# Kernel tuning notes

Measured on AMD Instinct MI355X. Metric: run time of the kernel, lower is better.

The kernel has to match this reference:

```python
import jax, jax.numpy as jnp
import numpy as np


def setup_inputs() -> dict:
    key = jax.random.key(0)
    ks = jax.random.split(key, 4)
    B, S, D, E = 8, 4096, 2048, 64
    scale = 1.0 / np.sqrt(D)
    return {
        "x": jax.random.normal(ks[0], (B, S, D), dtype=jnp.float32),
        "W_route": jax.random.normal(ks[1], (E, D), dtype=jnp.float32) * scale,
        "b_route": jnp.zeros((E,), dtype=jnp.float32),
        "W_noise": jax.random.normal(ks[2], (E, D), dtype=jnp.float32) * scale,
        "b_noise": jnp.zeros((E,), dtype=jnp.float32),
        "noise_eps": jax.random.normal(ks[3], (B, S, E), dtype=jnp.float32),
    }


TOP_K = 2


def reference(x, W_route, b_route, W_noise, b_noise, noise_eps):
    # Dual linear projections: [B,S,D] @ [D,E] -> [B,S,E]
    logits = jnp.einsum("bsd,ed->bse", x, W_route) + b_route
    noise_logits = jnp.einsum("bsd,ed->bse", x, W_noise) + b_noise
    noisy_logits = logits + noise_eps * jax.nn.softplus(noise_logits)

    B, S, E = noisy_logits.shape
    flat = noisy_logits.reshape(B * S, E)
    top_vals, top_idx = jax.lax.top_k(flat, TOP_K)  # [N,K]

    # Scatter top-k values into -inf background, then softmax over experts.
    neg_inf = jnp.full_like(flat, -jnp.inf)
    rows = jnp.arange(B * S)[:, None]
    sparse = neg_inf.at[rows, top_idx].set(top_vals)
    router_output = jax.nn.softmax(sparse, axis=-1).reshape(B, S, E)
    indices = top_idx.reshape(B, S, TOP_K)
    return router_output, indices
```

## Files before the change

### kernel.cpp

```cpp
#include <hip/hip_runtime.h>
#include <math.h>

typedef _Float16 f16;
typedef __attribute__((ext_vector_type(8))) _Float16 half8;
typedef __attribute__((ext_vector_type(4))) float f32x4;

#define NEXP 64
#define TM 64
#define L_STRIDE 132

__device__ __forceinline__ float softplus_f(float x) {
    return fmaxf(x, 0.0f) + log1pf(expf(-fabsf(x)));
}

__device__ __forceinline__ void lds_dma16(const void* g, void* l) {
    __builtin_amdgcn_global_load_lds(
        (const __attribute__((address_space(1))) unsigned int*)g,
        (__attribute__((address_space(3))) unsigned int*)l, 16, 0, 0);
}

__global__ void wsplit_kernel(const float* __restrict__ Wr,
                              const float* __restrict__ Wn,
                              f16* __restrict__ ws, int D) {
    const int per_col = D >> 3;
    const int t = blockIdx.x * blockDim.x + threadIdx.x;
    const int col = t / per_col;
    const int k0  = (t - col * per_col) * 8;
    if (col >= 128) return;
    const float* src = (col < NEXP) ? &Wr[(size_t)col * D] : &Wn[(size_t)(col - NEXP) * D];
    const float4 v0 = *(const float4*)&src[k0];
    const float4 v1 = *(const float4*)&src[k0 + 4];
    const float vv[8] = {v0.x, v0.y, v0.z, v0.w, v1.x, v1.y, v1.z, v1.w};
    half8 hi, lo;
#pragma unroll
    for (int j = 0; j < 8; ++j) {
        const f16 h = (f16)vv[j];
        hi[j] = h;
        lo[j] = (f16)((vv[j] - (float)h) * 4096.0f);
    }
    const int kc = k0 >> 5, q = (k0 >> 3) & 3;
    const size_t base = (size_t)kc * 8192 + (size_t)q * 1024 + (size_t)col * 8;
    *(half8*)&ws[base]        = hi;
    *(half8*)&ws[base + 4096] = lo;
}

__global__ __launch_bounds__(256, 2)
void router_mfma_kernel(const float* __restrict__ x,
                        const f16* __restrict__ wsW,
                        const float* __restrict__ br,
                        const float* __restrict__ bn,
                        const float* __restrict__ eps,
                        float* __restrict__ out,
                        int N, int D) {
    __shared__ union alignas(16) {
        struct {
            f16 B[2][4][128][8];
            f16 A[2][4][64][8];
        } st;
        float L[TM][L_STRIDE];
    } sm;
    __shared__ float biasLDS[128];
    __shared__ float p1s[TM], p2s[TM];
    __shared__ int   i1s[TM], i2s[TM];

    const int tid  = threadIdx.x;
    const int lane = tid & 63;
    const int w    = tid >> 6;
    const int rowbase = blockIdx.x * TM;
    const int wr = w & 1, wc = w >> 1;
    const int quad = lane >> 4;
    const int l16  = lane & 15;

    if (tid < 128) biasLDS[tid] = (tid < NEXP) ? br[tid] : bn[tid - NEXP];

    f32x4 accM[2][4], accC[2][4];
#pragma unroll
    for (int i = 0; i < 2; ++i)
#pragma unroll
        for (int j = 0; j < 4; ++j) {
            accM[i][j] = (f32x4){0.f, 0.f, 0.f, 0.f};
            accC[i][j] = (f32x4){0.f, 0.f, 0.f, 0.f};
        }

    const int sr = tid >> 2;
    const int sq = tid & 3;
    const float* xrow = &x[(size_t)(rowbase + sr) * D + sq * 8];

    const int nkc = D >> 5;
    float4 v0 = *(const float4*)&xrow[0];
    float4 v1 = *(const float4*)&xrow[4];

    for (int kc = 0; kc < nkc; ++kc) {
        {
            const char* gsrc = (const char*)wsW + (size_t)kc * 16384 + w * 4096 + lane * 16;
            char* ldst = (char*)&sm.st.B[0][0][0][0] + w * 4096;
#pragma unroll
            for (int i = 0; i < 4; ++i)
                lds_dma16(gsrc + i * 1024, ldst + i * 1024);
        }
        {
            const float vv[8] = {v0.x, v0.y, v0.z, v0.w, v1.x, v1.y, v1.z, v1.w};
            half8 hv, lv;
#pragma unroll
            for (int j = 0; j < 8; ++j) {
                const f16 h = (f16)vv[j];
                hv[j] = h;
                lv[j] = (f16)((vv[j] - (float)h) * 4096.0f);
            }
            *(half8*)&sm.st.A[0][sq][sr][0] = hv;
            *(half8*)&sm.st.A[1][sq][sr][0] = lv;
        }
        __syncthreads();

        half8 ah[2], al[2], bh[4], bl[4];
#pragma unroll
        for (int rt = 0; rt < 2; ++rt) {
            ah[rt] = *(const half8*)&sm.st.A[0][quad][wr * 32 + rt * 16 + l16][0];
            al[rt] = *(const half8*)&sm.st.A[1][quad][wr * 32 + rt * 16 + l16][0];
        }
#pragma unroll
        for (int ct = 0; ct < 4; ++ct) {
            bh[ct] = *(const half8*)&sm.st.B[0][quad][wc * 64 + ct * 16 + l16][0];
            bl[ct] = *(const half8*)&sm.st.B[1][quad][wc * 64 + ct * 16 + l16][0];
        }

        const int kn = (kc + 1 < nkc) ? kc + 1 : kc;
        v0 = *(const float4*)&xrow[kn * 32];
        v1 = *(const float4*)&xrow[kn * 32 + 4];

#pragma unroll
        for (int rt = 0; rt < 2; ++rt)
#pragma unroll
            for (int ct = 0; ct < 4; ++ct) {
                accM[rt][ct] = __builtin_amdgcn_mfma_f32_16x16x32_f16(ah[rt], bh[ct], accM[rt][ct], 0, 0, 0);
                accC[rt][ct] = __builtin_amdgcn_mfma_f32_16x16x32_f16(al[rt], bh[ct], accC[rt][ct], 0, 0, 0);
                accC[rt][ct] = __builtin_amdgcn_mfma_f32_16x16x32_f16(ah[rt], bl[ct], accC[rt][ct], 0, 0, 0);
            }
        __syncthreads();
    }

#pragma unroll
    for (int rt = 0; rt < 2; ++rt)
#pragma unroll
        for (int ct = 0; ct < 4; ++ct) {
            const int row = wr * 32 + rt * 16 + quad * 4;
            const int col = wc * 64 + ct * 16 + l16;
            const float bcol = biasLDS[col];
#pragma unroll
            for (int rg = 0; rg < 4; ++rg)
                sm.L[row + rg][col] = accM[rt][ct][rg] + accC[rt][ct][rg] * (1.0f / 4096.0f) + bcol;
        }
    __syncthreads();

#pragma unroll
    for (int t = 0; t < 4; ++t) {
        const int f   = tid * 4 + t * 1024;
        const int row = f >> 6;
        const int e0  = f & 63;
        const float4 ev = *(const float4*)&eps[(size_t)(rowbase + row) * NEXP + e0];
        const float evs[4] = {ev.x, ev.y, ev.z, ev.w};
#pragma unroll
        for (int j = 0; j < 4; ++j) {
            const float lg = sm.L[row][e0 + j];
            const float nz = sm.L[row][NEXP + e0 + j];
            sm.L[row][e0 + j] = fmaf(evs[j], softplus_f(nz), lg);
        }
    }
    __syncthreads();

    if (tid < TM) {
        const int r = tid;
        float v1t = -INFINITY, v2t = -INFINITY;
        int i1 = 0, i2 = 0;
#pragma unroll 8
        for (int e = 0; e < NEXP; ++e) {
            const float v = sm.L[r][e];
            if (v > v1t) { v2t = v1t; i2 = i1; v1t = v; i1 = e; }
            else if (v > v2t) { v2t = v; i2 = e; }
        }
        const float z = expf(v2t - v1t);
        const float s = 1.0f + z;
        p1s[r] = 1.0f / s;
        p2s[r] = z / s;
        i1s[r] = i1;
        i2s[r] = i2;
        float* oidx = out + (size_t)N * NEXP + (size_t)(rowbase + r) * 2;
        oidx[0] = (float)i1;
        oidx[1] = (float)i2;
    }
    __syncthreads();

    {
        const int r = tid >> 2;
        const int g = tid & 3;
        const float pa = p1s[r], pb = p2s[r];
        const int i1 = i1s[r], i2 = i2s[r];
        float* orow = out + (size_t)(rowbase + r) * NEXP;
#pragma unroll
        for (int t = 0; t < 4; ++t) {
            const int e0 = g * 16 + t * 4;
            float4 o;
            o.x = (e0 + 0 == i1) ? pa : ((e0 + 0 == i2) ? pb : 0.0f);
            o.y = (e0 + 1 == i1) ? pa : ((e0 + 1 == i2) ? pb : 0.0f);
            o.z = (e0 + 2 == i1) ? pa : ((e0 + 2 == i2) ? pb : 0.0f);
            o.w = (e0 + 3 == i1) ? pa : ((e0 + 3 == i2) ? pb : 0.0f);
            *(float4*)&orow[e0] = o;
        }
    }
}

#define BK 32
#define XS_STRIDE (TM + 4)
#define WS_STRIDE (128 + 4)

__global__ __launch_bounds__(256, 2)
void noisy_topk_router_kernel(const float* __restrict__ x,
                              const float* __restrict__ Wr,
                              const float* __restrict__ br,
                              const float* __restrict__ Wn,
                              const float* __restrict__ bn,
                              const float* __restrict__ eps,
                              float* __restrict__ out,
                              int N, int D) {
    __shared__ union alignas(16) {
        struct {
            float Xs[BK][XS_STRIDE];
            float Ws[BK][WS_STRIDE];
        } st;
        float L[TM][L_STRIDE];
    } sm;
    __shared__ float p1s[TM], p2s[TM];
    __shared__ int   i1s[TM], i2s[TM];

    const int tid = threadIdx.x;
    const int rowbase = blockIdx.x * TM;
    const int r0 = (tid >> 5) * 8;
    const int c0 = (tid & 31) * 4;

    float acc[8][4];
#pragma unroll
    for (int i = 0; i < 8; ++i)
#pragma unroll
        for (int j = 0; j < 4; ++j) acc[i][j] = 0.0f;

    const int q  = tid & 7;
    const int rr = tid >> 3;

    for (int k0 = 0; k0 < D; k0 += BK) {
#pragma unroll
        for (int i = 0; i < 2; ++i) {
            const int row = rr + 32 * i;
            const float4 xv = *(const float4*)&x[(size_t)(rowbase + row) * D + k0 + q * 4];
            sm.st.Xs[q * 4 + 0][row] = xv.x;
            sm.st.Xs[q * 4 + 1][row] = xv.y;
            sm.st.Xs[q * 4 + 2][row] = xv.z;
            sm.st.Xs[q * 4 + 3][row] = xv.w;
            const float4 wv = *(const float4*)&Wr[(size_t)row * D + k0 + q * 4];
            sm.st.Ws[q * 4 + 0][row] = wv.x;
            sm.st.Ws[q * 4 + 1][row] = wv.y;
            sm.st.Ws[q * 4 + 2][row] = wv.z;
            sm.st.Ws[q * 4 + 3][row] = wv.w;
            const float4 nv = *(const float4*)&Wn[(size_t)row * D + k0 + q * 4];
            sm.st.Ws[q * 4 + 0][NEXP + row] = nv.x;
            sm.st.Ws[q * 4 + 1][NEXP + row] = nv.y;
            sm.st.Ws[q * 4 + 2][NEXP + row] = nv.z;
            sm.st.Ws[q * 4 + 3][NEXP + row] = nv.w;
        }
        __syncthreads();
#pragma unroll 4
        for (int kk = 0; kk < BK; ++kk) {
            const float4 xa = *(const float4*)&sm.st.Xs[kk][r0];
            const float4 xb = *(const float4*)&sm.st.Xs[kk][r0 + 4];
            const float4 wv = *(const float4*)&sm.st.Ws[kk][c0];
            const float xs[8] = {xa.x, xa.y, xa.z, xa.w, xb.x, xb.y, xb.z, xb.w};
            const float ws[4] = {wv.x, wv.y, wv.z, wv.w};
#pragma unroll
            for (int i = 0; i < 8; ++i)
#pragma unroll
                for (int j = 0; j < 4; ++j)
                    acc[i][j] = fmaf(xs[i], ws[j], acc[i][j]);
        }
        __syncthreads();
    }
    {
        const float4 bv = (c0 < NEXP) ? *(const float4*)&br[c0]
                                      : *(const float4*)&bn[c0 - NEXP];
#pragma unroll
        for (int i = 0; i < 8; ++i) {
            float4 o;
            o.x = acc[i][0] + bv.x;
            o.y = acc[i][1] + bv.y;
            o.z = acc[i][2] + bv.z;
            o.w = acc[i][3] + bv.w;
            *(float4*)&sm.L[r0 + i][c0] = o;
        }
    }
    __syncthreads();
#pragma unroll
    for (int t = 0; t < 4; ++t) {
        const int f   = tid * 4 + t * 1024;
        const int row = f >> 6;
        const int e0  = f & 63;
        const float4 ev = *(const float4*)&eps[(size_t)(rowbase + row) * NEXP + e0];
        const float evs[4] = {ev.x, ev.y, ev.z, ev.w};
#pragma unroll
        for (int j = 0; j < 4; ++j) {
            const float lg = sm.L[row][e0 + j];
            const float nz = sm.L[row][NEXP + e0 + j];
            sm.L[row][e0 + j] = fmaf(evs[j], softplus_f(nz), lg);
        }
    }
    __syncthreads();
    if (tid < TM) {
        const int r = tid;
        float v1 = -INFINITY, v2 = -INFINITY;
        int i1 = 0, i2 = 0;
#pragma unroll 8
        for (int e = 0; e < NEXP; ++e) {
            const float v = sm.L[r][e];
            if (v > v1) { v2 = v1; i2 = i1; v1 = v; i1 = e; }
            else if (v > v2) { v2 = v; i2 = e; }
        }
        const float z = expf(v2 - v1);
        const float s = 1.0f + z;
        p1s[r] = 1.0f / s;
        p2s[r] = z / s;
        i1s[r] = i1;
        i2s[r] = i2;
        float* oidx = out + (size_t)N * NEXP + (size_t)(rowbase + r) * 2;
        oidx[0] = (float)i1;
        oidx[1] = (float)i2;
    }
    __syncthreads();
    {
        const int r = tid >> 2;
        const int g = tid & 3;
        const float pa = p1s[r], pb = p2s[r];
        const int i1 = i1s[r], i2 = i2s[r];
        float* orow = out + (size_t)(rowbase + r) * NEXP;
#pragma unroll
        for (int t = 0; t < 4; ++t) {
            const int e0 = g * 16 + t * 4;
            float4 o;
            o.x = (e0 + 0 == i1) ? pa : ((e0 + 0 == i2) ? pb : 0.0f);
            o.y = (e0 + 1 == i1) ? pa : ((e0 + 1 == i2) ? pb : 0.0f);
            o.z = (e0 + 2 == i1) ? pa : ((e0 + 2 == i2) ? pb : 0.0f);
            o.w = (e0 + 3 == i1) ? pa : ((e0 + 3 == i2) ? pb : 0.0f);
            *(float4*)&orow[e0] = o;
        }
    }
}

extern "C" void kernel_launch(void* const* d_in, const int* in_sizes, int n_in,
                              void* d_out, int out_size, void* d_ws, size_t ws_size,
                              hipStream_t stream) {
    const float* x   = (const float*)d_in[0];
    const float* Wr  = (const float*)d_in[1];
    const float* br  = (const float*)d_in[2];
    const float* Wn  = (const float*)d_in[3];
    const float* bn  = (const float*)d_in[4];
    const float* eps = (const float*)d_in[5];
    float* out = (float*)d_out;

    const int E = in_sizes[2];
    const int D = in_sizes[1] / E;
    const int N = in_sizes[0] / D;

    const size_t ws_needed = (size_t)128 * D * 2 * sizeof(f16);
    const bool fast = (E == 64) && (D == 2048) && (N % TM == 0) && (ws_size >= ws_needed);

    if (fast) {
        const int pre_threads = 128 * (D / 8);
        wsplit_kernel<<<(pre_threads + 255) / 256, 256, 0, stream>>>(Wr, Wn, (f16*)d_ws, D);
        router_mfma_kernel<<<N / TM, 256, 0, stream>>>(x, (const f16*)d_ws, br, bn, eps, out, N, D);
    } else {
        noisy_topk_router_kernel<<<N / TM, 256, 0, stream>>>(x, Wr, br, Wn, bn, eps, out, N, D);
    }
}
```

Before: 429.7 us.

## Double-buffer LDS staging of weights and x tiles in router MFMA loop

Converts the single-buffered LDS staging of weight (via global_load_lds) and split-fp16 x tiles into a ping-pong double buffer. The next k-chunk is issued before the current chunk's MFMAs, and x loads are prefetched two chunks ahead, so memory latency can overlap compute with fewer stalls per iteration. It also raises launch bounds to 3 blocks per CU and unrolls the loop by 2. The risks are more register pressure from the occupancy hint, and a sync pattern that may be incomplete because the remainder of the loop body is not visible.

```diff
diff --git a/kernel.cpp b/kernel.cpp
--- a/kernel.cpp
+++ b/kernel.cpp
@@ -17,6 +17,17 @@
     __builtin_amdgcn_global_load_lds(
         (const __attribute__((address_space(1))) unsigned int*)g,
         (__attribute__((address_space(3))) unsigned int*)l, 16, 0, 0);
+}
+
+__device__ __forceinline__ void cvt_split(const float4 a, const float4 b,
+                                          half8& hv, half8& lv) {
+    const float vv[8] = {a.x, a.y, a.z, a.w, b.x, b.y, b.z, b.w};
+#pragma unroll
+    for (int j = 0; j < 8; ++j) {
+        const f16 h = (f16)vv[j];
+        hv[j] = h;
+        lv[j] = (f16)((vv[j] - (float)h) * 4096.0f);
+    }
 }
 
 __global__ void wsplit_kernel(const float* __restrict__ Wr,
@@ -30,21 +41,15 @@
     const float* src = (col < NEXP) ? &Wr[(size_t)col * D] : &Wn[(size_t)(col - NEXP) * D];
     const float4 v0 = *(const float4*)&src[k0];
     const float4 v1 = *(const float4*)&src[k0 + 4];
-    const float vv[8] = {v0.x, v0.y, v0.z, v0.w, v1.x, v1.y, v1.z, v1.w};
     half8 hi, lo;
-#pragma unroll
-    for (int j = 0; j < 8; ++j) {
-        const f16 h = (f16)vv[j];
-        hi[j] = h;
-        lo[j] = (f16)((vv[j] - (float)h) * 4096.0f);
-    }
+    cvt_split(v0, v1, hi, lo);
     const int kc = k0 >> 5, q = (k0 >> 3) & 3;
     const size_t base = (size_t)kc * 8192 + (size_t)q * 1024 + (size_t)col * 8;
     *(half8*)&ws[base]        = hi;
     *(half8*)&ws[base + 4096] = lo;
 }
 
-__global__ __launch_bounds__(256, 2)
+__global__ __launch_bounds__(256, 3)
 void router_mfma_kernel(const float* __restrict__ x,
                         const f16* __restrict__ wsW,
                         const float* __restrict__ br,
@@ -53,10 +58,7 @@
                         float* __restrict__ out,
                         int N, int D) {
     __shared__ union alignas(16) {
-        struct {
-            f16 B[2][4][128][8];
-            f16 A[2][4][64][8];
-        } st;
+        struct { f16 B[2][8192]; f16 A[2][4096]; } st;
         float L[TM][L_STRIDE];
     } sm;
     __shared__ float biasLDS[128];
@@ -85,48 +87,56 @@
     const int sr = tid >> 2;
     const int sq = tid & 3;
     const float* xrow = &x[(size_t)(rowbase + sr) * D + sq * 8];
-
     const int nkc = D >> 5;
-    float4 v0 = *(const float4*)&xrow[0];
-    float4 v1 = *(const float4*)&xrow[4];
-
+
+    {
+        const char* gsrc = (const char*)wsW + (size_t)0 * 16384 + w * 4096 + lane * 16;
+        char* ldst = (char*)&sm.st.B[0][0] + w * 4096;
+#pragma unroll
+        for (int i = 0; i < 4; ++i) lds_dma16(gsrc + i * 1024, ldst + i * 1024);
+        const float4 a0 = *(const float4*)&xrow[0];
+        const float4 a1 = *(const float4*)&xrow[4];
+        half8 hv, lv;
+        cvt_split(a0, a1, hv, lv);
+        *(half8*)&sm.st.A[0][sq * 512 + sr * 8]        = hv;
+        *(half8*)&sm.st.A[0][2048 + sq * 512 + sr * 8] = lv;
+    }
+    float4 v0 = *(const float4*)&xrow[32];
+    float4 v1 = *(const float4*)&xrow[36];
+    __syncthreads();
+
+#pragma unroll 2
     for (int kc = 0; kc < nkc; ++kc) {
-        {
-            const char* gsrc = (const char*)wsW + (size_t)kc * 16384 + w * 4096 + lane * 16;
-            char* ldst = (char*)&sm.st.B[0][0][0][0] + w * 4096;
-#pragma unroll
-            for (int i = 0; i < 4; ++i)
-                lds_dma16(gsrc + i * 1024, ldst + i * 1024);
-        }
-        {
-            const float vv[8] = {v0.x, v0.y, v0.z, v0.w, v1.x, v1.y, v1.z, v1.w};
+        const int cur = kc & 1, nxt = cur ^ 1;
+
+        if (kc + 1 < nkc) {
+            const char* gsrc = (const char*)wsW + (size_t)(kc + 1) * 16384 + w * 4096 + lane * 16;
+            char* ldst = (char*)&sm.st.B[nxt][0] + w * 4096;
+#pragma unroll
+            for (int i = 0; i < 4; ++i) lds_dma16(gsrc + i * 1024, ldst + i * 1024);
             half8 hv, lv;
-#pragma unroll
-            for (int j = 0; j < 8; ++j) {
-                const f16 h = (f16)vv[j];
-                hv[j] = h;
-                lv[j] = (f16)((vv[j] - (float)h) * 4096.0f);
-            }
-            *(half8*)&sm.st.A[0][sq][sr][0] = hv;
-            *(half8*)&sm.st.A[1][sq][sr][0] = lv;
-        }
-        __syncthreads();
+            cvt_split(v0, v1, hv, lv);
+            *(half8*)&sm.st.A[nxt][sq * 512 + sr * 8]        = hv;
+            *(half8*)&sm.st.A[nxt][2048 + sq * 512 + sr * 8] = lv;
+        }
+        if (kc + 2 < nkc) {
+            v0 = *(const float4*)&xrow[(kc + 2) * 32];
+            v1 = *(const float4*)&xrow[(kc + 2) * 32 + 4];
+        }
 
         half8 ah[2], al[2], bh[4], bl[4];
 #pragma unroll
         for (int rt = 0; rt < 2; ++rt) {
-            ah[rt] = *(const half8*)&sm.st.A[0][quad][wr * 32 + rt * 16 + l16][0];
-            al[rt] = *(const half8*)&sm.st.A[1][quad][wr * 32 + rt * 16 + l16][0];
+            const int r = (wr * 32 + rt * 16 + l16) * 8;
+            ah[rt] = *(const half8*)&sm.st.A[cur][quad * 512 + r];
+            al[rt] = *(const half8*)&sm.st.A[cur][2048 + quad * 512 + r];
         }
 #pragma unroll
         for (int ct = 0; ct < 4; ++ct) {
-            bh[ct] = *(const half8*)&sm.st.B[0][quad][wc * 64 + ct * 16 + l16][0];
-            bl[ct] = *(const half8*)&sm.st.B[1][quad][wc * 64 + ct * 16 + l16][0];
-        }
-
-        const int kn = (kc + 1 < nkc) ? kc + 1 : kc;
-        v0 = *(const float4*)&xrow[kn * 32];
-        v1 = *(const float4*)&xrow[kn * 32 + 4];
+            const int c = (wc * 64 + ct * 16 + l16) * 8;
+            bh[ct] = *(const half8*)&sm.st.B[cur][quad * 1024 + c];
+            bl[ct] = *(const half8*)&sm.st.B[cur][4096 + quad * 1024 + c];
+        }
 
 #pragma unroll
         for (int rt = 0; rt < 2; ++rt)
```

Result: no change. 429.0 us (-0.2%).
